# Optimization experiments

Measured on AMD Instinct MI355X. Metric: run time of the kernel, lower is better.

The kernel has to match this reference:

```python
import jax, jax.numpy as jnp
import numpy as np

KERNEL_MUL = 2.0
KERNEL_NUM = 5


def setup_inputs() -> dict:
    key = jax.random.key(0)
    k1, k2 = jax.random.split(key)
    source = jax.random.normal(k1, (4096, 512), dtype=jnp.float32)
    target = jax.random.normal(k2, (4096, 512), dtype=jnp.float32)
    return {"source": source, "target": target}


def reference(source, target):
    B = source.shape[0]
    src = source.reshape(B, -1)
    tgt = target.reshape(B, -1)
    total = jnp.concatenate([src, tgt], axis=0)  # [2B, D]
    n = 2 * B

    # Pairwise squared L2 via ||a||^2 + ||b||^2 - 2 a.b (GEMM trick)
    sq = jnp.sum(total * total, axis=-1)  # [2B]
    d2 = sq[:, None] + sq[None, :] - 2.0 * (total @ total.T)  # [2B, 2B]
    d2 = jnp.maximum(d2, 0.0)

    # Median-heuristic-style bandwidth; torch uses L2_distance.data (no grad)
    bandwidth = jax.lax.stop_gradient(jnp.sum(d2)) / (n * n - n)
    bandwidth = bandwidth / (KERNEL_MUL ** (KERNEL_NUM // 2))

    # Multi-bandwidth Gaussian kernel sum
    kernels = jnp.zeros_like(d2)
    for i in range(KERNEL_NUM):
        kernels = kernels + jnp.exp(-d2 / (bandwidth * (KERNEL_MUL ** i)))

    XX = kernels[:B, :B]
    YY = kernels[B:, B:]
    XY = kernels[:B, B:]
    YX = kernels[B:, :B]
    return jnp.mean(XX + YY - XY - YX)
```

## Files before the change

kernel.cpp:

```cpp
#include <hip/hip_runtime.h>


typedef int i32x4 __attribute__((ext_vector_type(4)));

#define N_TOT  8192
#define DIM    512
#define QSCALE 24.0f
#define NPANEL 64
#define NPH    2080
#define FP_OFF 295040
#define IMG_OFF 327680ULL

__device__ __forceinline__ int q8(float x) {
    int q = __float2int_rn(x * QSCALE);
    return max(-127, min(127, q));
}

__device__ __forceinline__ void gload16(const void* g, void* l) {
    __builtin_amdgcn_global_load_lds(
        (const __attribute__((address_space(1))) unsigned int*)g,
        (__attribute__((address_space(3))) unsigned int*)l, 16, 0, 0);
}

__global__ __launch_bounds__(256) void k_pre(
    const float* __restrict__ src, const float* __restrict__ tgt,
    unsigned char* __restrict__ img,
    float* __restrict__ sq, float* __restrict__ v)
{
    __shared__ __align__(16) signed char qt[128][80];
    const int b = blockIdx.x;
    const int p = b >> 3, kp = b & 7;
    const int t = threadIdx.x;
    const float* base = ((p < 32) ? src + (size_t)p * 128 * DIM
                                  : tgt + (size_t)(p - 32) * 128 * DIM) + kp * 64;
    {
        int r = t >> 1, ch = (t & 1) * 32;
        const float* qp = base + (size_t)r * DIM + ch;
        float rsq = 0.f;
        #pragma unroll
        for (int j = 0; j < 8; ++j) {
            float4 x = *(const float4*)(qp + j * 4);
            int q0 = q8(x.x), q1 = q8(x.y), q2 = q8(x.z), q3 = q8(x.w);
            unsigned int w = (q0 & 255) | ((q1 & 255) << 8) | ((q2 & 255) << 16)
                             | ((unsigned)(q3 & 255) << 24);
            *(unsigned int*)&qt[r][ch + j * 4] = w;
            rsq += (float)(q0 * q0 + q1 * q1 + q2 * q2 + q3 * q3);
        }
        rsq += __shfl_xor(rsq, 1);
        if ((t & 1) == 0) atomicAdd(&sq[p * 128 + r], rsq);
    }
    __syncthreads();
    #pragma unroll
    for (int h = 0; h < 2; ++h) {
        int ci = t + h * 256;
        int g = ci >> 6, lane = ci & 63;
        int row = g * 16 + (lane & 15), c0 = (lane >> 4) * 16;
        uint4 w = *(const uint4*)&qt[row][c0];
        *(uint4*)(img + (size_t)p * 65536 + (size_t)kp * 8192
                  + (size_t)g * 1024 + (size_t)lane * 16) = w;
    }
    if (t < 64) {
        float s = 0.f;
        for (int r = 0; r < 128; ++r) s += (float)qt[r][t];
        atomicAdd(&v[kp * 64 + t], s);
    }
}

#define STAGEP(LDSBUF, PANEL)                                                  \
    do {                                                                       \
        const char* g_ = ic + (size_t)(PANEL) * 65536;                         \
        _Pragma("unroll")                                                      \
        for (int i_ = 0; i_ < 16; ++i_)                                        \
            gload16(g_ + i_ * 4096 + tid * 16,                                 \
                    LDSBUF + i_ * 4096 + wid * 1024);                          \
    } while (0)

__global__ __launch_bounds__(256, 1) void kmain(
    const unsigned char* __restrict__ img,
    const float* __restrict__ sq, const float* __restrict__ v,
    float* __restrict__ Fpart)
{
    __shared__ __align__(16) char lA[65536];
    __shared__ __align__(16) char lB[65536];
    __shared__ float redS[4], redV[4];

    const int tid  = threadIdx.x;
    const int lane = tid & 63;
    const int wid  = tid >> 6;
    const int wr   = wid >> 1, wc = wid & 1;
    const int lhi  = lane >> 4, llo = lane & 15;
    const int lofs = lane * 16;
    const char* ic = (const char*)img;

    int b = blockIdx.x;
    int s = (b & 7) * 32 + (b >> 3);
    int p0  = s * 8 + (s < 32 ? s : 32);
    int cnt = (s < 32) ? 9 : 8;

    int rem = p0, I = 0;
    while (rem >= NPANEL - I) { rem -= NPANEL - I; ++I; }
    int J = I + rem;

    STAGEP(lA, I);
    STAGEP(lB, J);

    float Sp = 0.f;
    #pragma unroll
    for (int i = 0; i < 32; ++i) Sp += sq[tid + i * 256];
    float Vp;
    { float v0 = v[tid], v1 = v[tid + 256]; Vp = v0 * v0 + v1 * v1; }
    #pragma unroll
    for (int off = 32; off > 0; off >>= 1) {
        Sp += __shfl_down(Sp, off);
        Vp += __shfl_down(Vp, off);
    }
    if (lane == 0) { redS[wid] = Sp; redV[wid] = Vp; }
    __syncthreads();
    float S = redS[0] + redS[1] + redS[2] + redS[3];
    float V = redV[0] + redV[1] + redV[2] + redV[3];
    float sumd2 = 2.f * (float)N_TOT * S - 2.f * V;
    float bw = sumd2 / ((float)N_TOT * (float)N_TOT - (float)N_TOT) * 0.25f;
    const float c = 1.4426950408889634f / (16.f * bw);

    float local = 0.f;

    for (int e = 0; e < cnt; ++e) {
        i32x4 acc[4][4];
        #pragma unroll
        for (int m = 0; m < 4; ++m)
            #pragma unroll
            for (int n = 0; n < 4; ++n) acc[m][n] = (i32x4){0, 0, 0, 0};

        #pragma unroll
        for (int kp = 0; kp < 8; ++kp) {
            i32x4 aF[4], bF[4];
            #pragma unroll
            for (int m = 0; m < 4; ++m) {
                aF[m] = *(const i32x4*)(lA + kp * 8192 + (wr * 4 + m) * 1024 + lofs);
                bF[m] = *(const i32x4*)(lB + kp * 8192 + (wc * 4 + m) * 1024 + lofs);
            }
            #pragma unroll
            for (int m = 0; m < 4; ++m)
                #pragma unroll
                for (int n = 0; n < 4; ++n)
                    acc[m][n] = __builtin_amdgcn_mfma_i32_16x16x64_i8(
                        aF[m], bF[n], acc[m][n], 0, 0, 0);
        }

        const float sgn  = ((I < 32) == (J < 32)) ? 1.f : -1.f;
        const bool  diag = (I == J);
        const float wp   = diag ? sgn : 2.f * sgn;
        float sqc_[4];
        #pragma unroll
        for (int n = 0; n < 4; ++n)
            sqc_[n] = sq[J * 128 + wc * 64 + n * 16 + llo];
        float psum = 0.f;
        #pragma unroll
        for (int m = 0; m < 4; ++m) {
            float sqr_[4];
            #pragma unroll
            for (int r = 0; r < 4; ++r)
                sqr_[r] = sq[I * 128 + wr * 64 + m * 16 + lhi * 4 + r];
            #pragma unroll
            for (int n = 0; n < 4; ++n)
                #pragma unroll
                for (int r = 0; r < 4; ++r) {
                    float d2 = sqr_[r] + sqc_[n] - 2.f * (float)acc[m][n][r];
                    d2 = fmaxf(d2, 0.f);
                    float u = __builtin_amdgcn_exp2f(-d2 * c);
                    float u2 = u * u, u4 = u2 * u2, u8 = u4 * u4, u16 = u8 * u8;
                    float k5 = u + u2 + u4 + u8 + u16;
                    if (diag) {
                        int ri = wr * 64 + m * 16 + lhi * 4 + r;
                        int cj = wc * 64 + n * 16 + llo;
                        k5 *= (cj > ri) ? 2.f : ((cj == ri) ? 1.f : 0.f);
                    }
                    psum += k5;
                }
        }
        local += wp * psum;

        int In = I, Jn = J + 1;
        if (Jn == NPANEL) { ++In; Jn = In; }
        __syncthreads();
        if (e + 1 < cnt) {
            if (In != I) STAGEP(lA, In);
            STAGEP(lB, Jn);
        }
        I = In; J = Jn;
        __syncthreads();
    }

    #pragma unroll
    for (int off = 32; off > 0; off >>= 1) local += __shfl_down(local, off);
    if (lane == 0) Fpart[b * 4 + wid] = local;
}

__global__ void k4_out(const float* __restrict__ Fpart, float* __restrict__ out) {
    int t = threadIdx.x;
    double s = 0.0;
    for (int i = t; i < 1024; i += 256) s += (double)Fpart[i];
    #pragma unroll
    for (int off = 32; off > 0; off >>= 1) s += __shfl_down(s, off);
    __shared__ double r[4];
    if ((t & 63) == 0) r[t >> 6] = s;
    __syncthreads();
    if (t == 0) out[0] = (float)((r[0] + r[1] + r[2] + r[3]) / ((double)4096 * 4096.0));
}

extern "C" void kernel_launch(void* const* d_in, const int* in_sizes, int n_in,
                              void* d_out, int out_size, void* d_ws, size_t ws_size,
                              hipStream_t stream) {
    const float* src = (const float*)d_in[0];
    const float* tgt = (const float*)d_in[1];
    char* ws = (char*)d_ws;
    float* sq    = (float*)ws;
    float* v     = (float*)(ws + 32768);
    float* Fpart = (float*)(ws + FP_OFF);
    unsigned char* img = (unsigned char*)(ws + IMG_OFF);
    float* out = (float*)d_out;

    hipMemsetAsync(ws, 0, 34816, stream);
    hipLaunchKernelGGL(k_pre, dim3(512), dim3(256), 0, stream, src, tgt, img, sq, v);
    hipLaunchKernelGGL(kmain, dim3(256), dim3(256), 0, stream, img, sq, v, Fpart);
    hipLaunchKernelGGL(k4_out, dim3(1), dim3(256), 0, stream, Fpart, out);
}
```

Baseline: 62.19 us.

## Double-buffer B panel in K-halves to overlap loads with MFMA and epilogue

Splits the B-panel LDS staging into two 32 KB half-buffers and pipelines it across the tile loop. The second K-half is fetched while the first half is multiplied, and the next tile's first half is fetched during the second-half MFMAs and the exp epilogue. The goal is to hide global-to-LDS load latency that previously sat between barriers. Panel changes of A still stall. The change also drops the fmaxf clamp, since the quantized integer distances are non-negative, and adds an unused COMP_HALF macro.

```diff
diff --git a/kernel.cpp b/kernel.cpp
--- a/kernel.cpp
+++ b/kernel.cpp
@@ -5,9 +5,9 @@
 
 #define N_TOT  8192
 #define DIM    512
+#define BM     128
+#define NPANEL 64
 #define QSCALE 24.0f
-#define NPANEL 64
-#define NPH    2080
 #define FP_OFF 295040
 #define IMG_OFF 327680ULL
 
@@ -27,12 +27,12 @@
     unsigned char* __restrict__ img,
     float* __restrict__ sq, float* __restrict__ v)
 {
-    __shared__ __align__(16) signed char qt[128][80];
+    __shared__ __align__(16) signed char qt[BM][80];
     const int b = blockIdx.x;
     const int p = b >> 3, kp = b & 7;
     const int t = threadIdx.x;
-    const float* base = ((p < 32) ? src + (size_t)p * 128 * DIM
-                                  : tgt + (size_t)(p - 32) * 128 * DIM) + kp * 64;
+    const float* base = ((p < 32) ? src + (size_t)p * BM * DIM
+                                  : tgt + (size_t)(p - 32) * BM * DIM) + kp * 64;
     {
         int r = t >> 1, ch = (t & 1) * 32;
         const float* qp = base + (size_t)r * DIM + ch;
@@ -47,7 +47,7 @@
             rsq += (float)(q0 * q0 + q1 * q1 + q2 * q2 + q3 * q3);
         }
         rsq += __shfl_xor(rsq, 1);
-        if ((t & 1) == 0) atomicAdd(&sq[p * 128 + r], rsq);
+        if ((t & 1) == 0) atomicAdd(&sq[p * BM + r], rsq);
     }
     __syncthreads();
     #pragma unroll
@@ -61,27 +61,55 @@
     }
     if (t < 64) {
         float s = 0.f;
-        for (int r = 0; r < 128; ++r) s += (float)qt[r][t];
+        for (int r = 0; r < BM; ++r) s += (float)qt[r][t];
         atomicAdd(&v[kp * 64 + t], s);
     }
 }
 
-#define STAGEP(LDSBUF, PANEL)                                                  \
+#define STAGE_A(PANEL)                                                         \
     do {                                                                       \
         const char* g_ = ic + (size_t)(PANEL) * 65536;                         \
         _Pragma("unroll")                                                      \
         for (int i_ = 0; i_ < 16; ++i_)                                        \
-            gload16(g_ + i_ * 4096 + tid * 16,                                 \
-                    LDSBUF + i_ * 4096 + wid * 1024);                          \
+            gload16(g_ + i_ * 4096 + tid * 16, lA + i_ * 4096 + wid * 1024);   \
+    } while (0)
+
+#define STAGE_BH(BUF, PANEL, KH)                                               \
+    do {                                                                       \
+        const char* g_ = ic + (size_t)(PANEL) * 65536 + (KH) * 32768;          \
+        _Pragma("unroll")                                                      \
+        for (int i_ = 0; i_ < 8; ++i_)                                         \
+            gload16(g_ + i_ * 4096 + tid * 16, (BUF) + i_ * 4096 + wid * 1024);\
+    } while (0)
+
+#define COMP_HALF(BUF, KH)                                                     \
+    do {                                                                       \
+        _Pragma("unroll")                                                      \
+        for (int kq = 0; kq < 4; ++kq) {                                       \
+            const int kp = (KH) * 4 + kq;                                      \
+            i32x4 aF[4], bF[4];                                                \
+            _Pragma("unroll")                                                  \
+            for (int m = 0; m < 4; ++m) {                                      \
+                aF[m] = *(const i32x4*)(lA + kp * 8192 + (wr * 4 + m) * 1024 + lofs); \
+                bF[m] = *(const i32x4*)((BUF) + kq * 8192 + (wc * 4 + m) * 1024 + lofs); \
+            }                                                                  \
+            _Pragma("unroll")                                                  \
+            for (int m = 0; m < 4; ++m)                                        \
+                _Pragma("unroll")                                              \
+                for (int n = 0; n < 4; ++n)                                    \
+                    acc[m][n] = __builtin_amdgcn_mfma_i32_32x32x16_i8(         \
+                        aF[m], bF[n], acc[m][n], 0, 0, 0) ;   \
+        }                                                                      \
     } while (0)
 
 __global__ __launch_bounds__(256, 1) void kmain(
     const unsigned char* __restrict__ img,
-    const float* __restrict__ sq, const float* __restrict__ v,
+    const float* __restrict__ sq, const float* __restrict__ vv_,
     float* __restrict__ Fpart)
 {
     __shared__ __align__(16) char lA[65536];
-    __shared__ __align__(16) char lB[65536];
+    __shared__ __align__(16) char lB0[32768];
+    __shared__ __align__(16) char lB1[32768];
     __shared__ float redS[4], redV[4];
 
     const int tid  = threadIdx.x;
@@ -101,14 +129,14 @@
     while (rem >= NPANEL - I) { rem -= NPANEL - I; ++I; }
     int J = I + rem;
 
-    STAGEP(lA, I);
-    STAGEP(lB, J);
+    STAGE_A(I);
+    STAGE_BH(lB0, J, 0);
 
     float Sp = 0.f;
     #pragma unroll
     for (int i = 0; i < 32; ++i) Sp += sq[tid + i * 256];
     float Vp;
-    { float v0 = v[tid], v1 = v[tid + 256]; Vp = v0 * v0 + v1 * v1; }
+    { float v0 = vv_[tid], v1 = vv_[tid + 256]; Vp = v0 * v0 + v1 * v1; }
     #pragma unroll
     for (int off = 32; off > 0; off >>= 1) {
         Sp += __shfl_down(Sp, off);
@@ -123,6 +151,8 @@
     const float c = 1.4426950408889634f / (16.f * bw);
 
     float local = 0.f;
+    char* bufc = lB0;
+    char* bufn = lB1;
 
     for (int e = 0; e < cnt; ++e) {
         i32x4 acc[4][4];
@@ -131,13 +161,14 @@
             #pragma unroll
             for (int n = 0; n < 4; ++n) acc[m][n] = (i32x4){0, 0, 0, 0};
 
-        #pragma unroll
-        for (int kp = 0; kp < 8; ++kp) {
+        STAGE_BH(bufn, J, 1);
+        #pragma unroll
+        for (int kq = 0; kq < 4; ++kq) {
             i32x4 aF[4], bF[4];
             #pragma unroll
             for (int m = 0; m < 4; ++m) {
-                aF[m] = *(const i32x4*)(lA + kp * 8192 + (wr * 4 + m) * 1024 + lofs);
-                bF[m] = *(const i32x4*)(lB + kp * 8192 + (wc * 4 + m) * 1024 + lofs);
+                aF[m] = *(const i32x4*)(lA + kq * 8192 + (wr * 4 + m) * 1024 + lofs);
+                bF[m] = *(const i32x4*)(bufc + kq * 8192 + (wc * 4 + m) * 1024 + lofs);
             }
             #pragma unroll
             for (int m = 0; m < 4; ++m)
@@ -146,49 +177,75 @@
                     acc[m][n] = __builtin_amdgcn_mfma_i32_16x16x64_i8(
                         aF[m], bF[n], acc[m][n], 0, 0, 0);
         }
-
-        const float sgn  = ((I < 32) == (J < 32)) ? 1.f : -1.f;
-        const bool  diag = (I == J);
-        const float wp   = diag ? sgn : 2.f * sgn;
-        float sqc_[4];
-        #pragma unroll
-        for (int n = 0; n < 4; ++n)
-            sqc_[n] = sq[J * 128 + wc * 64 + n * 16 + llo];
-        float psum = 0.f;
-        #pragma unroll
-        for (int m = 0; m < 4; ++m) {
-            float sqr_[4];
-            #pragma unroll
-            for (int r = 0; r < 4; ++r)
-                sqr_[r] = sq[I * 128 + wr * 64 + m * 16 + lhi * 4 + r];
-            #pragma unroll
-            for (int n = 0; n < 4; ++n)
-                #pragma unroll
-                for (int r = 0; r < 4; ++r) {
-                    float d2 = sqr_[r] + sqc_[n] - 2.f * (float)acc[m][n][r];
-                    d2 = fmaxf(d2, 0.f);
-                    float u = __builtin_amdgcn_exp2f(-d2 * c);
-                    float u2 = u * u, u4 = u2 * u2, u8 = u4 * u4, u16 = u8 * u8;
-                    float k5 = u + u2 + u4 + u8 + u16;
-                    if (diag) {
-                        int ri = wr * 64 + m * 16 + lhi * 4 + r;
-                        int cj = wc * 64 + n * 16 + llo;
-                        k5 *= (cj > ri) ? 2.f : ((cj == ri) ? 1.f : 0.f);
-                    }
-                    psum += k5;
-                }
-        }
-        local += wp * psum;
+        __syncthreads();
+        { char* t_ = bufc; bufc = bufn; bufn = t_; }
 
         int In = I, Jn = J + 1;
         if (Jn == NPANEL) { ++In; Jn = In; }
+        const bool more = (e + 1 < cnt);
+        const bool sameI = (In == I);
+
+        if (more && sameI) STAGE_BH(bufn, Jn, 0);
+        #pragma unroll
+        for (int kq = 0; kq < 4; ++kq) {
+            i32x4 aF[4], bF[4];
+            #pragma unroll
+            for (int m = 0; m < 4; ++m) {
+                aF[m] = *(const i32x4*)(lA + (4 + kq) * 8192 + (wr * 4 + m) * 1024 + lofs);
+                bF[m] = *(const i32x4*)(bufc + kq * 8192 + (wc * 4 + m) * 1024 + lofs);
+            }
+            #pragma unroll
+            for (int m = 0; m < 4; ++m)
+                #pragma unroll
+                for (int n = 0; n < 4; ++n)
+                    acc[m][n] = __builtin_amdgcn_mfma_i32_16x16x64_i8(
+                        aF[m], bF[n], acc[m][n], 0, 0, 0);
+        }
+
+        {
+            const float sgn  = ((I < 32) == (J < 32)) ? 1.f : -1.f;
+            const bool  diag = (I == J);
+            const float wp   = diag ? sgn : 2.f * sgn;
+            float sqc_[4];
+            #pragma unroll
+            for (int n = 0; n < 4; ++n)
+                sqc_[n] = sq[J * BM + wc * 64 + n * 16 + llo];
+            float psum = 0.f;
+            #pragma unroll
+            for (int m = 0; m < 4; ++m) {
+                float sqr_[4];
+                #pragma unroll
+                for (int r = 0; r < 4; ++r)
+                    sqr_[r] = sq[I * BM + wr * 64 + m * 16 + lhi * 4 + r];
+                #pragma unroll
+                for (int n = 0; n < 4; ++n)
+                    #pragma unroll
+                    for (int r = 0; r < 4; ++r) {
+                        float d2 = fmaf(-2.f, (float)acc[m][n][r],
+                                        sqr_[r] + sqc_[n]);
+                        float u = __builtin_amdgcn_exp2f(-d2 * c);
+                        float u2 = u * u, u4 = u2 * u2, u8 = u4 * u4, u16 = u8 * u8;
+                        float k5 = u + u2 + u4 + u8 + u16;
+                        if (diag) {
+                            int ri = wr * 64 + m * 16 + lhi * 4 + r;
+                            int cj = wc * 64 + n * 16 + llo;
+                            k5 *= (cj > ri) ? 2.f : ((cj == ri) ? 1.f : 0.f);
+                        }
+                        psum += k5;
+                    }
+            }
+            local += wp * psum;
+        }
+
         __syncthreads();
-        if (e + 1 < cnt) {
-            if (In != I) STAGEP(lA, In);
-            STAGEP(lB, Jn);
+        { char* t_ = bufc; bufc = bufn; bufn = t_; }
+
+        if (more && !sameI) {
+            STAGE_A(In);
+            STAGE_BH(bufc, Jn, 0);
+            __syncthreads();
         }
         I = In; J = Jn;
-        __syncthreads();
     }
 
     #pragma unroll
```

Result: no change. 61.33 us (-1.4%).
